# Kernel tuning notes

Hardware: AMD Instinct MI355X
Metric: run time of the kernel (lower is better)

The kernel has to match this reference:

```python
import jax, jax.numpy as jnp
import numpy as np

B, L, K, NRBF = 2, 2048, 32, 16
NODE_F, EDGE_F = 128, 128
MAX_REL = 32  # af2 relpos -> 2*32+1 = 65 bins
NODE_IN, EDGE_IN = 21 + 6 + 8, 65 + 25 * NRBF + 1 + 2


def _ln(x, g, b, eps=1e-5):
    mu = jnp.mean(x, -1, keepdims=True)
    var = jnp.var(x, -1, keepdims=True)
    return (x - mu) / jnp.sqrt(var + eps) * g + b


def _normalize(t):
    return jnp.nan_to_num(t / jnp.linalg.norm(t, axis=-1, keepdims=True))


def _dihedral(p0, p1, p2, p3):
    u0, u1, u2 = p2 - p1, p0 - p1, p3 - p2
    n1 = _normalize(jnp.cross(u0, u1))
    n2 = _normalize(jnp.cross(u0, u2))
    sgn = jnp.sign(jnp.sum(jnp.cross(u1, u2) * u0, -1))
    return jnp.nan_to_num(sgn * jnp.arccos(jnp.sum(n1 * n2, -1)))


def setup_inputs() -> dict:
    key = jax.random.key(0)
    ks = jax.random.split(key, 9)
    return {
        "X": jax.random.normal(ks[0], (B, L, 4, 3), jnp.float32) * 5.0,
        "S": jax.random.randint(ks[1], (B, L), 0, 21),
        "BB_D_sincos": jax.random.normal(ks[2], (B, L, 3, 2), jnp.float32),
        "SC_D_sincos": jax.random.normal(ks[3], (B, L, 4, 2), jnp.float32),
        "chain_indices": jax.random.randint(ks[4], (B, L), 0, 2),
        "mask": jnp.ones((B, L), jnp.float32),
        "W_node": jax.random.normal(ks[5], (NODE_IN, NODE_F), jnp.float32) * 0.05,
        "b_node": jnp.zeros((NODE_F,), jnp.float32),
        "g_node": jnp.ones((NODE_F,), jnp.float32),
        "beta_node": jnp.zeros((NODE_F,), jnp.float32),
        "W_edge": jax.random.normal(ks[6], (EDGE_IN, EDGE_F), jnp.float32) * 0.05,
        "b_edge": jnp.zeros((EDGE_F,), jnp.float32),
        "g_edge": jnp.ones((EDGE_F,), jnp.float32),
        "beta_edge": jnp.zeros((EDGE_F,), jnp.float32),
    }


def reference(X, S, BB_D_sincos, SC_D_sincos, chain_indices, mask,
              W_node, b_node, g_node, beta_node,
              W_edge, b_edge, g_edge, beta_edge):
    Bn, Ln = X.shape[:2]
    N, Ca, C, O = X[:, :, 0], X[:, :, 1], X[:, :, 2], X[:, :, 3]
    # ---- masked pairwise Ca distances + kNN topk (smallest) ----
    m2 = mask[:, None, :] * mask[:, :, None]                      # [B,L,L]
    dX = Ca[:, :, None, :] - Ca[:, None, :, :]
    D = m2 * jnp.sqrt(jnp.sum(dX * dX, -1) + 1e-6)
    D_adj = D + 2.0 * (1.0 - m2) * jnp.max(D, -1, keepdims=True)
    _, E_idx = jax.lax.top_k(-D_adj, K)                           # [B,L,K]
    bidx = jnp.arange(Bn)[:, None, None]
    # ---- af2 relative-position one-hot (residue_index=None path) ----
    offset = E_idx - jnp.arange(Ln)[None, :, None]
    E_pos = jax.nn.one_hot(jnp.clip(offset + MAX_REL, 0, 2 * MAX_REL),
                           2 * MAX_REL + 1, dtype=jnp.float32)    # [B,L,K,65]
    # ---- impute CB, 5x5 atomic-distance RBFs at neighbors only ----
    bv, cv = Ca - N, C - Ca
    Cb = -0.58273431 * jnp.cross(bv, cv) + 0.56802827 * bv - 0.54067466 * cv + Ca
    X5 = jnp.stack((N, Ca, C, O, Cb), axis=-2)                    # [B,L,5,3]
    X5_nb = X5[bidx, E_idx]                                       # [B,L,K,5,3]
    dA = X5[:, :, None, :, None, :] - X5_nb[:, :, :, None, :, :]  # [B,L,K,5i,5j,3]
    Dn = jnp.sqrt(jnp.sum(dA * dA, -1) + 1e-6)                    # [B,L,K,5,5]
    mu = jnp.linspace(0.0, 20.0, NRBF)
    sigma = 20.0 / NRBF
    RBF_all = jnp.exp(-(((Dn[..., None] - mu) / sigma) ** 2))
    RBF_all = RBF_all.reshape(Bn, Ln, K, 25 * NRBF)               # i-major, j, rbf order
    # ---- edge type: same-chain indicator + 1 ----
    ch_nb = chain_indices[bidx, E_idx]
    E_type = ((ch_nb == chain_indices[:, :, None]).astype(jnp.float32) + 1.0)[..., None]
    # ---- pairwise dihedrals, evaluated only at neighbors ----
    N_nb, Ca_nb, C_nb = N[bidx, E_idx], Ca[bidx, E_idx], C[bidx, E_idx]
    ir_phi = _dihedral(C[:, :, None, :], N_nb, Ca_nb, C_nb)
    ir_psi = _dihedral(N[:, :, None, :], Ca[:, :, None, :], C[:, :, None, :], N_nb)
    dihed = jnp.stack((ir_phi, ir_psi), -1)                       # [B,L,K,2]
    # ---- fuse + embed ----
    E = jnp.concatenate((E_pos, RBF_all, E_type, dihed), -1)      # [B,L,K,468]
    V = jnp.concatenate((jax.nn.one_hot(S, 21, dtype=jnp.float32),
                         BB_D_sincos.reshape(Bn, Ln, -1),
                         SC_D_sincos.reshape(Bn, Ln, -1)), -1)    # [B,L,35]
    h_V = _ln(V @ W_node + b_node, g_node, beta_node)
    h_E = _ln(E @ W_edge + b_edge, g_edge, beta_edge)
    return (h_V, h_E, E_idx, X)
```

## Files before the change

### kernel.cpp

```cpp
#include <hip/hip_runtime.h>
#include <math.h>

#define NB 2
#define NL 2048
#define NK 32
#define NODE_F 128
#define EDGE_F 128

#define OFF_HV   0
#define OFF_HE   (NB*NL*NODE_F)
#define OFF_EIDX (OFF_HE + NB*NL*NK*EDGE_F)
#define OFF_X    (OFF_EIDX + NB*NL*NK)

#define ACH 8
#define BCH 8
#define SAW 264
#define NCH 16

typedef __attribute__((ext_vector_type(8))) short v8s;
typedef __attribute__((ext_vector_type(4))) float v4f;

__device__ __forceinline__ short f2bf(float f) {
    unsigned u = __float_as_uint(f);
    unsigned r = u + 0x7fffu + ((u >> 16) & 1u);
    return (short)(r >> 16);
}

#if __has_builtin(__builtin_amdgcn_exp2f)
#define EXP2F(x) __builtin_amdgcn_exp2f(x)
#else
#define EXP2F(x) __expf((x) * 0.6931471805599453f)
#endif

__device__ __forceinline__ unsigned bfpack(float f0, float f1) {
    unsigned u0 = __float_as_uint(f0), u1 = __float_as_uint(f1);
#if __has_builtin(__builtin_amdgcn_perm)
    return __builtin_amdgcn_perm(u1, u0, 0x07060302u);
#else
    return (u1 & 0xFFFF0000u) | (u0 >> 16);
#endif
}

template<int CTRL>
__device__ __forceinline__ float dpp_add_f32(float x) {
    int p = __builtin_amdgcn_update_dpp(0, __float_as_int(x), CTRL, 0xF, 0xF, true);
    return x + __int_as_float(p);
}
template<int CTRL>
__device__ __forceinline__ float dpp_max_f32(float x) {
    int p = __builtin_amdgcn_update_dpp(0, __float_as_int(x), CTRL, 0xF, 0xF, true);
    return fmaxf(x, __int_as_float(p));
}
__device__ __forceinline__ float dpp_row_sum16(float x) {
    x = dpp_add_f32<0x111>(x);
    x = dpp_add_f32<0x112>(x);
    x = dpp_add_f32<0x114>(x);
    x = dpp_add_f32<0x118>(x);
    return x;
}
__device__ __forceinline__ float dpp_wave_sum(float x) {
    x = dpp_row_sum16(x);
    x = dpp_add_f32<0x142>(x);
    x = dpp_add_f32<0x143>(x);
    return __int_as_float(__builtin_amdgcn_readlane(__float_as_int(x), 63));
}
__device__ __forceinline__ float dpp_wave_max_nn(float x) {
    x = dpp_max_f32<0x111>(x);
    x = dpp_max_f32<0x112>(x);
    x = dpp_max_f32<0x114>(x);
    x = dpp_max_f32<0x118>(x);
    x = dpp_max_f32<0x142>(x);
    x = dpp_max_f32<0x143>(x);
    return __int_as_float(__builtin_amdgcn_readlane(__float_as_int(x), 63));
}

template<int CTRL>
__device__ __forceinline__ unsigned dpp_min_u32_step(unsigned x) {
    unsigned p = (unsigned)__builtin_amdgcn_update_dpp((int)x, (int)x, CTRL, 0xF, 0xF, false);
    return p < x ? p : x;
}
__device__ __forceinline__ unsigned wave_min_u32_dpp(unsigned x) {
    x = dpp_min_u32_step<0xB1>(x);
    x = dpp_min_u32_step<0x4E>(x);
    x = dpp_min_u32_step<0x141>(x);
    x = dpp_min_u32_step<0x140>(x);
    x = dpp_min_u32_step<0x142>(x);
    x = dpp_min_u32_step<0x143>(x);
    return x;
}

__device__ __forceinline__ void cross3(const float a[3], const float b[3], float c[3]) {
    c[0] = a[1]*b[2] - a[2]*b[1];
    c[1] = a[2]*b[0] - a[0]*b[2];
    c[2] = a[0]*b[1] - a[1]*b[0];
}
__device__ __forceinline__ float dot3(const float a[3], const float b[3]) {
    return a[0]*b[0] + a[1]*b[1] + a[2]*b[2];
}
__device__ float dihedral_f(const float p0[3], const float p1[3],
                            const float p2[3], const float p3[3]) {
    float u0[3], u1[3], u2[3];
    for (int d = 0; d < 3; d++) {
        u0[d] = p2[d] - p1[d];
        u1[d] = p0[d] - p1[d];
        u2[d] = p3[d] - p2[d];
    }
    float n1[3], n2[3], c12[3];
    cross3(u0, u1, n1);
    cross3(u0, u2, n2);
    cross3(u1, u2, c12);
    float l1 = sqrtf(dot3(n1, n1));
    float l2 = sqrtf(dot3(n2, n2));
    float cosang = dot3(n1, n2) / (l1 * l2);
    float s = dot3(c12, u0);
    float sgn = (s > 0.f) ? 1.f : ((s < 0.f) ? -1.f : 0.f);
    float r = sgn * acosf(cosang);
    return isnan(r) ? 0.f : r;
}

__global__ __launch_bounds__(256) void fused_pre_kernel(const float* __restrict__ X,
                                                        const float* __restrict__ mask,
                                                        const int* __restrict__ S,
                                                        const float* __restrict__ BB,
                                                        const float* __restrict__ SC,
                                                        const float* __restrict__ Wn,
                                                        const float* __restrict__ bn,
                                                        const float* __restrict__ gn,
                                                        const float* __restrict__ betan,
                                                        const float* __restrict__ We,
                                                        const float* __restrict__ be,
                                                        float* __restrict__ X5,
                                                        short* __restrict__ WTf,
                                                        int* __restrict__ EidxW,
                                                        float* __restrict__ out) {
    __shared__ float sCa[NL * 3];
    __shared__ unsigned long long sSel[4][64];
    int blk = blockIdx.x;
    int tid = threadIdx.x;

    if (blk >= 1024) {
        if (blk < 1040) {
            int row = (blk - 1024) * 256 + tid;
            float v[12];
#pragma unroll
            for (int t = 0; t < 12; t++) v[t] = X[row * 12 + t];
#pragma unroll
            for (int t = 0; t < 12; t++) out[OFF_X + row * 12 + t] = v[t];
            float bv[3], cv[3], cr[3];
            for (int d = 0; d < 3; d++) { bv[d] = v[3+d] - v[d]; cv[d] = v[6+d] - v[3+d]; }
            cross3(bv, cv, cr);
            float* x5 = X5 + row * 15;
#pragma unroll
            for (int t = 0; t < 12; t++) x5[t] = v[t];
            for (int d = 0; d < 3; d++)
                x5[12 + d] = -0.58273431f * cr[d] + 0.56802827f * bv[d] - 0.54067466f * cv[d] + v[3+d];
        } else {
            int t = (blk - 1040) * 256 + tid;
            if (t >= NCH * 8 * 64) return;
            int lane = t & 63;
            int nt = (t >> 6) & 7;
            int ch = t >> 9;
            int n = nt * 16 + (lane & 15);
            int kbase = ch * 32 + (lane >> 4) * 8;
            short* dst = WTf + (size_t)t * 8;
#pragma unroll
            for (int j = 0; j < 8; j++) {
                int k = kbase + j;
                float f;
                if (k < 403) f = We[(65 + k) * 128 + n];
                else if (k == 403) f = be[n];
                else if (k <= 468) f = We[(k - 404) * 128 + n];
                else f = 0.f;
                dst[j] = f2bf(f);
            }
        }
        return;
    }

    int w = tid >> 6, l = tid & 63;
    int row = blk * 4 + w;
    int b = row / NL;
    int base = b * NL;

    for (int idx = tid; idx < NL; idx += 256) {
        const float* xp = X + (size_t)(base + idx) * 12 + 3;
        sCa[idx * 3 + 0] = xp[0];
        sCa[idx * 3 + 1] = xp[1];
        sCa[idx * 3 + 2] = xp[2];
    }

    {
        int f0 = l, f1 = 64 + l;
        int s = S[row];
        float a0 = bn[f0] + Wn[s * NODE_F + f0];
        float a1 = bn[f1] + Wn[s * NODE_F + f1];
#pragma unroll
        for (int t = 0; t < 6; t++) {
            float x = BB[row * 6 + t];
            a0 += x * Wn[(21 + t) * NODE_F + f0];
            a1 += x * Wn[(21 + t) * NODE_F + f1];
        }
#pragma unroll
        for (int t = 0; t < 8; t++) {
            float x = SC[row * 8 + t];
            a0 += x * Wn[(27 + t) * NODE_F + f0];
            a1 += x * Wn[(27 + t) * NODE_F + f1];
        }
        float tot = dpp_wave_sum(a0 + a1);
        float mean = tot * (1.0f / 128.0f);
        float d0 = a0 - mean, d1 = a1 - mean;
        float qt = dpp_wave_sum(d0 * d0 + d1 * d1);
        float rstd = 1.0f / sqrtf(qt * (1.0f / 128.0f) + 1e-5f);
        out[OFF_HV + row * NODE_F + f0] = d0 * rstd * gn[f0] + betan[f0];
        out[OFF_HV + row * NODE_F + f1] = d1 * rstd * gn[f1] + betan[f1];
    }
    __syncthreads();

    const float* mrow = mask + base;
    int lrow = row - base;
    float cx = sCa[lrow * 3 + 0], cy = sCa[lrow * 3 + 1], cz = sCa[lrow * 3 + 2];
    float mi = mrow[lrow];

    float K[32];
    float lmax = 0.0f;
#pragma unroll
    for (int t = 0; t < 32; t++) {
        int j = t * 64 + l;
        float dx = __fsub_rn(cx, sCa[j * 3 + 0]);
        float dy = __fsub_rn(cy, sCa[j * 3 + 1]);
        float dz = __fsub_rn(cz, sCa[j * 3 + 2]);
        float ss = __fadd_rn(__fadd_rn(__fadd_rn(__fmul_rn(dx, dx), __fmul_rn(dy, dy)),
                                       __fmul_rn(dz, dz)), 1e-6f);
        float d = __fmul_rn(__fmul_rn(mi, mrow[j]), __fsqrt_rn(ss));
        K[t] = d;
        lmax = fmaxf(lmax, d);
    }
    lmax = dpp_wave_max_nn(lmax);
#pragma unroll
    for (int t = 0; t < 32; t++) {
        int j = t * 64 + l;
        float m2 = __fmul_rn(mi, mrow[j]);
        K[t] = __fadd_rn(K[t], __fmul_rn(__fmul_rn(2.0f, __fsub_rn(1.0f, m2)), lmax));
    }

    unsigned lo_ = 0u, hi_ = 0x7f7fffffu, tau = 0x7f7fffffu;
#pragma unroll 1
    for (int it = 0; it < 31; it++) {
        unsigned mid = (lo_ + hi_) >> 1;
        float tf = __uint_as_float(mid);
        int c = 0;
#pragma unroll
        for (int t = 0; t < 32; t++) c += __popcll(__ballot(K[t] <= tf));
        if (c >= 32) {
            tau = mid;
            if (c <= 64) break;
            hi_ = mid - 1;
        } else {
            lo_ = mid + 1;
        }
    }
    float tauf = __uint_as_float(tau);

    sSel[w][l] = ~0ull;
    int cbase = 0;
#pragma unroll
    for (int t = 0; t < 32; t++) {
        bool q = (K[t] <= tauf);
        unsigned long long m = __ballot(q);
        int pos = cbase + __popcll(m & ((1ull << l) - 1ull));
        if (q && pos < 64)
            sSel[w][pos] = (((unsigned long long)__float_as_uint(K[t])) << 32)
                           | (unsigned)(t * 64 + l);
        cbase += __popcll(m);
    }

    unsigned long long key = sSel[w][l];
    int selj = 0;
#pragma unroll 1
    for (int r = 0; r < NK; r++) {
        unsigned hi = (unsigned)(key >> 32);
        unsigned gh = (unsigned)__builtin_amdgcn_readlane((int)wave_min_u32_dpp(hi), 63);
        unsigned long long mask_ = __ballot(hi == gh);
        int wl = __ffsll((unsigned long long)mask_) - 1;
        unsigned j = (unsigned)__builtin_amdgcn_readlane((int)(unsigned)key, wl);
        if (l == r) selj = (int)j;
        if (l == wl) key = ~0ull;
    }
    if (l < NK) {
        EidxW[row * NK + l] = selj;
        out[OFF_EIDX + row * NK + l] = (float)selj;
    }
}

__global__ __launch_bounds__(256, 4) void edge10_kernel(const float* __restrict__ X5,
                                                        const int* __restrict__ Eidx,
                                                        const int* __restrict__ chain,
                                                        const float* __restrict__ ge,
                                                        const float* __restrict__ betae,
                                                        const short* __restrict__ WTf,
                                                        float* __restrict__ out) {
    __shared__ short sA[64 * SAW];
    __shared__ float sXj[64][17];
    __shared__ float sXi[2][15];
    __shared__ int   sJ[64];
    __shared__ int   sPos[64];
    __shared__ float sEt[64], sPhi[64], sPsi[64];

    int tid = threadIdx.x;
    int e0 = blockIdx.x * 64;
    int b = e0 / (NL * NK);
    int i0 = (e0 / NK) % NL;
    int lane = tid & 63, w = tid >> 6;

    if (tid < 64) sJ[tid] = Eidx[e0 + tid];
    if (tid < 30) sXi[tid / 15][tid % 15] = X5[(b * NL + i0 + tid / 15) * 15 + (tid % 15)];
    __syncthreads();

    for (int t = tid; t < 64 * 15; t += 256) {
        int e = t / 15, c2 = t % 15;
        sXj[e][c2] = X5[(b * NL + sJ[e]) * 15 + c2];
    }
    if (tid < 64) {
        int e = tid;
        int i = i0 + (e >> 5);
        int j = sJ[e];
        int off = j - i + 32;
        off = off < 0 ? 0 : (off > 64 ? 64 : off);
        sPos[e] = off;
        sEt[e] = (chain[b * NL + j] == chain[b * NL + i]) ? 2.0f : 1.0f;
    }
    __syncthreads();

    if (tid < 128) {
        int e = tid & 63;
        const float* xi = sXi[e >> 5];
        const float* xj = sXj[e];
        if (tid < 64) sPhi[e] = dihedral_f(&xi[6], &xj[0], &xj[3], &xj[6]);
        else          sPsi[e] = dihedral_f(&xi[0], &xi[3], &xi[6], &xj[0]);
    }

    const float Ac  = -0.92332482616893658f;
    const float K1c = 2.46219953645049755f;
    const float Rc  = EXP2F(-1.64146635763366503f);
    const float R2c = Rc * Rc;
    int eg_ = w * 16 + (lane & 15);
    int q_ = lane >> 4;
    const float* xiG = sXi[eg_ >> 5];
    const float* xjG = sXj[eg_];
    short* rowp = sA + eg_ * SAW;
    float hfq = (float)(q_ & 1);
    int posG = sPos[eg_];

#define SPECV(k) ((k) == 400 ? sEt[eg_] : (k) == 401 ? sPhi[eg_] : (k) == 402 ? sPsi[eg_] : \
                  (k) == 403 ? 1.0f : (((k) - 404 == posG) ? 1.0f : 0.0f))

#define GEN_A(hh, CNT)                                                         \
    {                                                                          \
        _Pragma("unroll")                                                      \
        for (int t = 0; t < (CNT); t++) {                                      \
            int o = q_ + t * 4;                                                \
            int kg = (hh) * 256 + o * 8;                                       \
            union { unsigned u[4]; v8s v; } au;                                \
            if (kg >= 400) {                                                   \
                _Pragma("unroll")                                              \
                for (int jp = 0; jp < 4; jp++) {                               \
                    int k0 = kg + 2 * jp;                                      \
                    au.u[jp] = bfpack(SPECV(k0), SPECV(k0 + 1));               \
                }                                                              \
            } else {                                                           \
                int pair = kg >> 4;                                            \
                int a = pair / 5, cc = pair - a * 5;                           \
                float dx = xiG[a*3+0] - xjG[cc*3+0];                           \
                float dy = xiG[a*3+1] - xjG[cc*3+1];                           \
                float dz = xiG[a*3+2] - xjG[cc*3+2];                           \
                float d = sqrtf(dx*dx + dy*dy + dz*dz + 1e-6f);                \
                float ee = fminf(__fmaf_rn(hfq, -10.666666666666666f, d), 40.f); \
                float r0 = EXP2F(Ac * ee * ee);                                \
                float g  = EXP2F(K1c * ee) * Rc;                               \
                float r1 = r0 * g; g *= R2c;                                   \
                float r2 = r1 * g; g *= R2c;                                   \
                float r3 = r2 * g; g *= R2c;                                   \
                float r4 = r3 * g; g *= R2c;                                   \
                float r5 = r4 * g; g *= R2c;                                   \
                float r6 = r5 * g; g *= R2c;                                   \
                float r7 = r6 * g;                                             \
                au.u[0] = bfpack(r0, r1);                                      \
                au.u[1] = bfpack(r2, r3);                                      \
                au.u[2] = bfpack(r4, r5);                                      \
                au.u[3] = bfpack(r6, r7);                                      \
            }                                                                  \
            *(v8s*)(rowp + o * 8) = au.v;                                      \
        }                                                                      \
    }

    GEN_A(0, ACH)
    __syncthreads();

    int cl = lane & 15, kq = lane >> 4;
    int ntA = 2 * w, ntB = ntA + 1;
    const char* sAc = (const char*)sA;
    int abase0 = cl * (SAW * 2) + kq * 16;

    v4f acc[4][2];
#pragma unroll
    for (int eg = 0; eg < 4; eg++) { acc[eg][0] = (v4f){0.f,0.f,0.f,0.f}; acc[eg][1] = (v4f){0.f,0.f,0.f,0.f}; }

#define MMA_HALF(CHBASE, CNT)                                                  \
    {                                                                          \
        _Pragma("unroll 2")                                                    \
        for (int chl = 0; chl < (CNT); chl++) {                                \
            const v8s* gb = (const v8s*)WTf + ((size_t)((CHBASE) + chl) * 512 + lane); \
            v8s b0 = gb[ntA * 64];                                             \
            v8s b1 = gb[ntB * 64];                                             \
            int ab = abase0 + chl * 64;                                        \
            v8s a0 = *(const v8s*)(sAc + ab);                                  \
            v8s a1 = *(const v8s*)(sAc + ab + 16 * (SAW * 2));                 \
            v8s a2 = *(const v8s*)(sAc + ab + 32 * (SAW * 2));                 \
            v8s a3 = *(const v8s*)(sAc + ab + 48 * (SAW * 2));                 \
            acc[0][0] = __builtin_amdgcn_mfma_f32_16x16x32_bf16(a0, b0, acc[0][0], 0, 0, 0); \
            acc[0][1] = __builtin_amdgcn_mfma_f32_16x16x32_bf16(a0, b1, acc[0][1], 0, 0, 0); \
            acc[1][0] = __builtin_amdgcn_mfma_f32_16x16x32_bf16(a1, b0, acc[1][0], 0, 0, 0); \
            acc[1][1] = __builtin_amdgcn_mfma_f32_16x16x32_bf16(a1, b1, acc[1][1], 0, 0, 0); \
            acc[2][0] = __builtin_amdgcn_mfma_f32_16x16x32_bf16(a2, b0, acc[2][0], 0, 0, 0); \
            acc[2][1] = __builtin_amdgcn_mfma_f32_16x16x32_bf16(a2, b1, acc[2][1], 0, 0, 0); \
            acc[3][0] = __builtin_amdgcn_mfma_f32_16x16x32_bf16(a3, b0, acc[3][0], 0, 0, 0); \
            acc[3][1] = __builtin_amdgcn_mfma_f32_16x16x32_bf16(a3, b1, acc[3][1], 0, 0, 0); \
        }                                                                      \
    }

    MMA_HALF(0, ACH)
    __syncthreads();
    GEN_A(1, BCH)
    __syncthreads();
    MMA_HALF(ACH, BCH)

    float2* sRed = (float2*)&sXj[0][0];
    int nA = ntA * 16 + cl, nB = nA + 16;
    float r4A = ge[nA], r5A = betae[nA];
    float r4B = ge[nB], r5B = betae[nB];

#pragma unroll
    for (int eg = 0; eg < 4; eg++) {
#pragma unroll
        for (int r = 0; r < 4; r++) {
            int e = eg * 16 + kq * 4 + r;
            float v0 = acc[eg][0][r];
            float v1 = acc[eg][1][r];
            float s  = dpp_row_sum16(v0 + v1);
            float q2 = dpp_row_sum16(v0 * v0 + v1 * v1);
            if (cl == 15) sRed[e * 4 + w] = make_float2(s, q2);
        }
    }
    __syncthreads();

#pragma unroll
    for (int eg = 0; eg < 4; eg++) {
#pragma unroll
        for (int r = 0; r < 4; r++) {
            int e = eg * 16 + kq * 4 + r;
            float4 pa = *(const float4*)&sRed[e * 4];
            float4 pb = *(const float4*)&sRed[e * 4 + 2];
            float s  = pa.x + pa.z + pb.x + pb.z;
            float q2 = pa.y + pa.w + pb.y + pb.w;
            float mean = s * (1.0f / 128.0f);
            float var = q2 * (1.0f / 128.0f) - mean * mean;
            float rstd = rsqrtf(var + 1e-5f);
            size_t base = OFF_HE + (size_t)(e0 + e) * 128;
            out[base + nA] = (acc[eg][0][r] - mean) * rstd * r4A + r5A;
            out[base + nB] = (acc[eg][1][r] - mean) * rstd * r4B + r5B;
        }
    }
}

extern "C" void kernel_launch(void* const* d_in, const int* in_sizes, int n_in,
                              void* d_out, int out_size, void* d_ws, size_t ws_size,
                              hipStream_t stream) {
    (void)in_sizes; (void)n_in; (void)out_size; (void)ws_size;
    const float* X    = (const float*)d_in[0];
    const int*   S    = (const int*)d_in[1];
    const float* BB   = (const float*)d_in[2];
    const float* SC   = (const float*)d_in[3];
    const int*   chain= (const int*)d_in[4];
    const float* mask = (const float*)d_in[5];
    const float* Wn   = (const float*)d_in[6];
    const float* bn   = (const float*)d_in[7];
    const float* gn   = (const float*)d_in[8];
    const float* betan= (const float*)d_in[9];
    const float* We   = (const float*)d_in[10];
    const float* be   = (const float*)d_in[11];
    const float* ge   = (const float*)d_in[12];
    const float* betae= (const float*)d_in[13];
    float* out = (float*)d_out;

    char* ws = (char*)d_ws;
    int*   EidxW = (int*)ws;
    float* X5    = (float*)(ws + 524288);
    short* WTf   = (short*)(ws + 770048);

    hipLaunchKernelGGL(fused_pre_kernel, dim3(1024 + 16 + 32), dim3(256), 0, stream,
                       X, mask, S, BB, SC, Wn, bn, gn, betan, We, be,
                       X5, WTf, EidxW, out);
    hipLaunchKernelGGL(edge10_kernel, dim3(NB * NL * NK / 64), dim3(256), 0, stream,
                       X5, EidxW, chain, ge, betae, WTf, out);
}
```

Measured before the change: 154.3 us.

## Replace serial top-K extraction with bitonic sort and compute full 16-RBF chains per thread

```diff
diff --git a/kernel.cpp b/kernel.cpp
--- a/kernel.cpp
+++ b/kernel.cpp
@@ -74,19 +74,23 @@
     return __int_as_float(__builtin_amdgcn_readlane(__float_as_int(x), 63));
 }
 
-template<int CTRL>
-__device__ __forceinline__ unsigned dpp_min_u32_step(unsigned x) {
-    unsigned p = (unsigned)__builtin_amdgcn_update_dpp((int)x, (int)x, CTRL, 0xF, 0xF, false);
-    return p < x ? p : x;
-}
-__device__ __forceinline__ unsigned wave_min_u32_dpp(unsigned x) {
-    x = dpp_min_u32_step<0xB1>(x);
-    x = dpp_min_u32_step<0x4E>(x);
-    x = dpp_min_u32_step<0x141>(x);
-    x = dpp_min_u32_step<0x140>(x);
-    x = dpp_min_u32_step<0x142>(x);
-    x = dpp_min_u32_step<0x143>(x);
-    return x;
+template<int J>
+__device__ __forceinline__ unsigned long long lane_xor64(unsigned long long x) {
+    if constexpr (J == 32) {
+        return __shfl_xor(x, 32, 64);
+    } else {
+        unsigned lo = (unsigned)x, hi = (unsigned)(x >> 32);
+        if constexpr (J == 1 || J == 2) {
+            constexpr int ctrl = (J == 1) ? 0xB1 : 0x4E;
+            lo = (unsigned)__builtin_amdgcn_update_dpp((int)lo, (int)lo, ctrl, 0xF, 0xF, false);
+            hi = (unsigned)__builtin_amdgcn_update_dpp((int)hi, (int)hi, ctrl, 0xF, 0xF, false);
+        } else {
+            constexpr int off = (J << 10) | 0x1F;
+            lo = (unsigned)__builtin_amdgcn_ds_swizzle((int)lo, off);
+            hi = (unsigned)__builtin_amdgcn_ds_swizzle((int)hi, off);
+        }
+        return (((unsigned long long)hi) << 32) | lo;
+    }
 }
 
 __device__ __forceinline__ void cross3(const float a[3], const float b[3], float c[3]) {
@@ -275,24 +279,27 @@
     }
 
     unsigned long long key = sSel[w][l];
-    int selj = 0;
-#pragma unroll 1
-    for (int r = 0; r < NK; r++) {
-        unsigned hi = (unsigned)(key >> 32);
-        unsigned gh = (unsigned)__builtin_amdgcn_readlane((int)wave_min_u32_dpp(hi), 63);
-        unsigned long long mask_ = __ballot(hi == gh);
-        int wl = __ffsll((unsigned long long)mask_) - 1;
-        unsigned j = (unsigned)__builtin_amdgcn_readlane((int)(unsigned)key, wl);
-        if (l == r) selj = (int)j;
-        if (l == wl) key = ~0ull;
-    }
+#define BSTAGE(K_, J_) {                                                       \
+    unsigned long long o_ = lane_xor64<J_>(key);                               \
+    bool keepMin = (((l & (K_)) == 0) == ((l & (J_)) == 0));                   \
+    unsigned long long mn_ = key < o_ ? key : o_;                              \
+    key = keepMin ? mn_ : (key ^ o_ ^ mn_);                                    \
+}
+    BSTAGE(2, 1)
+    BSTAGE(4, 2)  BSTAGE(4, 1)
+    BSTAGE(8, 4)  BSTAGE(8, 2)  BSTAGE(8, 1)
+    BSTAGE(16, 8) BSTAGE(16, 4) BSTAGE(16, 2) BSTAGE(16, 1)
+    BSTAGE(32, 16) BSTAGE(32, 8) BSTAGE(32, 4) BSTAGE(32, 2) BSTAGE(32, 1)
+    BSTAGE(64, 32) BSTAGE(64, 16) BSTAGE(64, 8) BSTAGE(64, 4) BSTAGE(64, 2) BSTAGE(64, 1)
+
     if (l < NK) {
+        int selj = (int)(unsigned)key;
         EidxW[row * NK + l] = selj;
         out[OFF_EIDX + row * NK + l] = (float)selj;
     }
 }
 
-__global__ __launch_bounds__(256, 4) void edge10_kernel(const float* __restrict__ X5,
+__global__ __launch_bounds__(256, 4) void edge11_kernel(const float* __restrict__ X5,
                                                         const int* __restrict__ Eidx,
                                                         const int* __restrict__ chain,
                                                         const float* __restrict__ ge,
@@ -348,52 +355,63 @@
     const float* xiG = sXi[eg_ >> 5];
     const float* xjG = sXj[eg_];
     short* rowp = sA + eg_ * SAW;
-    float hfq = (float)(q_ & 1);
     int posG = sPos[eg_];
 
 #define SPECV(k) ((k) == 400 ? sEt[eg_] : (k) == 401 ? sPhi[eg_] : (k) == 402 ? sPsi[eg_] : \
                   (k) == 403 ? 1.0f : (((k) - 404 == posG) ? 1.0f : 0.0f))
 
-#define GEN_A(hh, CNT)                                                         \
+#define GEN_A(hh)                                                              \
     {                                                                          \
         _Pragma("unroll")                                                      \
-        for (int t = 0; t < (CNT); t++) {                                      \
-            int o = q_ + t * 4;                                                \
-            int kg = (hh) * 256 + o * 8;                                       \
-            union { unsigned u[4]; v8s v; } au;                                \
-            if (kg >= 400) {                                                   \
+        for (int t = 0; t < 4; t++) {                                          \
+            int pl = q_ + t * 4;                         \
+            int p  = (hh) * 16 + pl;                          \
+            union { unsigned u[8]; v8s v[2]; } au;                             \
+            if ((hh) == 1 && p >= 25) {                                        \
                 _Pragma("unroll")                                              \
-                for (int jp = 0; jp < 4; jp++) {                               \
-                    int k0 = kg + 2 * jp;                                      \
+                for (int jp = 0; jp < 8; jp++) {                               \
+                    int k0 = p * 16 + 2 * jp;                                  \
                     au.u[jp] = bfpack(SPECV(k0), SPECV(k0 + 1));               \
                 }                                                              \
             } else {                                                           \
-                int pair = kg >> 4;                                            \
-                int a = pair / 5, cc = pair - a * 5;                           \
+                int a = p / 5, cc = p - a * 5;                                 \
                 float dx = xiG[a*3+0] - xjG[cc*3+0];                           \
                 float dy = xiG[a*3+1] - xjG[cc*3+1];                           \
                 float dz = xiG[a*3+2] - xjG[cc*3+2];                           \
                 float d = sqrtf(dx*dx + dy*dy + dz*dz + 1e-6f);                \
-                float ee = fminf(__fmaf_rn(hfq, -10.666666666666666f, d), 40.f); \
+                float ee = fminf(d, 40.f);                                     \
                 float r0 = EXP2F(Ac * ee * ee);                                \
                 float g  = EXP2F(K1c * ee) * Rc;                               \
-                float r1 = r0 * g; g *= R2c;                                   \
-                float r2 = r1 * g; g *= R2c;                                   \
-                float r3 = r2 * g; g *= R2c;                                   \
-                float r4 = r3 * g; g *= R2c;                                   \
-                float r5 = r4 * g; g *= R2c;                                   \
-                float r6 = r5 * g; g *= R2c;                                   \
-                float r7 = r6 * g;                                             \
-                au.u[0] = bfpack(r0, r1);                                      \
-                au.u[1] = bfpack(r2, r3);                                      \
-                au.u[2] = bfpack(r4, r5);                                      \
-                au.u[3] = bfpack(r6, r7);                                      \
+                float r1  = r0  * g; g *= R2c;                                 \
+                float r2  = r1  * g; g *= R2c;                                 \
+                float r3  = r2  * g; g *= R2c;                                 \
+                float r4  = r3  * g; g *= R2c;                                 \
+                float r5  = r4  * g; g *= R2c;                                 \
+                float r6  = r5  * g; g *= R2c;                                 \
+                float r7  = r6  * g; g *= R2c;                                 \
+                float r8  = r7  * g; g *= R2c;                                 \
+                float r9  = r8  * g; g *= R2c;                                 \
+                float r10 = r9  * g; g *= R2c;                                 \
+                float r11 = r10 * g; g *= R2c;                                 \
+                float r12 = r11 * g; g *= R2c;                                 \
+                float r13 = r12 * g; g *= R2c;                                 \
+                float r14 = r13 * g; g *= R2c;                                 \
+                float r15 = r14 * g;                                           \
+                au.u[0] = bfpack(r0,  r1);                                     \
+                au.u[1] = bfpack(r2,  r3);                                     \
+                au.u[2] = bfpack(r4,  r5);                                     \
+                au.u[3] = bfpack(r6,  r7);                                     \
+                au.u[4] = bfpack(r8,  r9);                                     \
+                au.u[5] = bfpack(r10, r11);                                    \
+                au.u[6] = bfpack(r12, r13);                                    \
+                au.u[7] = bfpack(r14, r15);                                    \
             }                                                                  \
-            *(v8s*)(rowp + o * 8) = au.v;                                      \
+            *(v8s*)(rowp + pl * 16)     = au.v[0];                             \
+            *(v8s*)(rowp + pl * 16 + 8) = au.v[1];                             \
         }                                                                      \
     }
 
-    GEN_A(0, ACH)
+    GEN_A(0)
     __syncthreads();
 
     int cl = lane & 15, kq = lane >> 4;
@@ -430,7 +448,7 @@
 
     MMA_HALF(0, ACH)
     __syncthreads();
-    GEN_A(1, BCH)
+    GEN_A(1)
     __syncthreads();
     MMA_HALF(ACH, BCH)
 
@@ -500,6 +518,6 @@
     hipLaunchKernelGGL(fused_pre_kernel, dim3(1024 + 16 + 32), dim3(256), 0, stream,
                        X, mask, S, BB, SC, Wn, bn, gn, betan, We, be,
                        X5, WTf, EidxW, out);
-    hipLaunchKernelGGL(edge10_kernel, dim3(NB * NL * NK / 64), dim3(256), 0, stream,
+    hipLaunchKernelGGL(edge11_kernel, dim3(NB * NL * NK / 64), dim3(256), 0, stream,
                        X5, EidxW, chain, ge, betae, WTf, out);
 }
```

Result: no change. 152.2 us (-1.4%).
